# Optimization experiments

Hardware: AMD Instinct MI355X
Metric: run time of the kernel (lower is better)

Reference implementation:

```python
import jax, jax.numpy as jnp
import numpy as np

EPS = 1e-8

def _normalize(x, eps=EPS):
    mean = jnp.mean(x, axis=-1, keepdims=True)
    var = jnp.var(x, axis=-1, keepdims=True)  # unbiased=False
    return (x - mean) / jnp.sqrt(var + eps)


def setup_inputs() -> dict:
    key = jax.random.key(0)
    ks = jax.random.split(key, 10)
    B, M, d = 8, 50000, 256
    out_units, num_heads, gsl_hidden = 256, 8, 16
    s = 0.02
    return {
        "h": jax.random.normal(ks[0], (B, M, d), dtype=jnp.float32),
        "att_w": jax.random.normal(ks[1], (d, num_heads), dtype=jnp.float32) * s,
        "att_b": jnp.zeros((num_heads,), dtype=jnp.float32),
        "w_w": jax.random.normal(ks[2], (d, out_units), dtype=jnp.float32) * s,
        "res_w": jax.random.normal(ks[3], (d, out_units), dtype=jnp.float32) * s,
        "res_b": jnp.zeros((out_units,), dtype=jnp.float32),
        "gsl1_w": jax.random.normal(ks[4], (d, gsl_hidden), dtype=jnp.float32) * s,
        "gsl1_b": jnp.zeros((gsl_hidden,), dtype=jnp.float32),
        "gsl2_w": jax.random.normal(ks[5], (gsl_hidden, 1), dtype=jnp.float32) * s,
        "gsl2_b": jnp.zeros((1,), dtype=jnp.float32),
        "k": 500,
    }


def reference(h, att_w, att_b, w_w, res_w, res_b, gsl1_w, gsl1_b, gsl2_w, gsl2_b, k):
    B, M, d = h.shape
    num_heads = att_w.shape[1]
    out_units = w_w.shape[1]
    head_dim = out_units // num_heads

    # additive attention scores per head: [B, M, H]
    A = jax.nn.relu(jnp.einsum('bmd,dh->bmh', h, att_w) + att_b)
    # value projection: [B, M, out]
    H_lin = jnp.einsum('bmd,de->bme', h, w_w)

    # learned graph-structure-learning scores: [B, M]
    S_hidden = jax.nn.relu(jnp.einsum('bmd,dg->bmg', h, gsl1_w) + gsl1_b)
    S = jax.nn.sigmoid(jnp.einsum('bmg,go->bmo', S_hidden, gsl2_w) + gsl2_b)[..., 0]

    # top-k mask over nodes (dim=1)
    k_eff = min(k, M)
    topk_vals, _ = jax.lax.top_k(S, k_eff)  # sorted descending
    kth = topk_vals[:, -1:]                 # [B, 1]
    mask = (S >= kth).astype(h.dtype)       # [B, M]

    # masked scores (zeros at masked positions, NOT -inf: faithful to source)
    A_mod = A * mask[:, :, None]            # [B, M, H]
    weights = jax.nn.softmax(A_mod, axis=1)  # softmax over M per head
    # (dropout is a no-op in eval mode)

    # per-head weighted sum over nodes, then concat heads along feature dim
    Hr = H_lin.reshape(B, M, num_heads, head_dim)
    out = jnp.einsum('bmh,bmhd->bhd', weights, Hr).reshape(B, 1, out_units)

    # residual from mean-pooled input
    Q_res = jax.nn.relu(jnp.einsum('bmd,de->bme', jnp.mean(h, axis=1, keepdims=True), res_w) + res_b)
    out = jax.nn.relu(out + Q_res)
    return _normalize(out), mask[:, None, :]
```

## Files before the change

kernel.cpp:

```cpp
#include <hip/hip_runtime.h>
#include <cstdint>
#include <cstddef>


#define MM     50000
#define BATCH  8
#define TILES  196
#define CANDCAP 4096
#define COMPCAP 2048

#define OFF_Z      0u
#define OFF_CANDR  1600000u
#define OFF_CANDK  1731072u
#define OFF_COMP   1993216u
#define OFF_LO     2058752u
#define OFF_PAD    2058784u
#define OFF_SUMH   2058848u
#define OFF_UCORR  2075232u
#define OFF_ZCORR  2206304u
#define OFF_CCNT   2206816u
#define OFF_CANDC  2206848u
#define ZERO_OFF   OFF_SUMH
#define ZERO_SZ    148032u

__device__ __forceinline__ unsigned int f32_sortable(float z) {
    unsigned int u = __float_as_uint(z);
    return (u & 0x80000000u) ? ~u : (u | 0x80000000u);
}

__global__ __launch_bounds__(256, 4) void k1_main(
    const float* __restrict__ h,
    const float* __restrict__ g1w,
    const float* __restrict__ g1b,
    const float* __restrict__ g2w,
    const float* __restrict__ g2b,
    float* __restrict__ z32,
    double* __restrict__ sumh)
{
    __shared__ float tile[4][16][66];
    __shared__ float lsum[256];
    __shared__ float wlds[256 * 16];

    const int tid  = threadIdx.x;
    const int w    = tid >> 6;
    const int lane = tid & 63;
    lsum[tid] = 0.0f;
    {
        const float4* g4 = (const float4*)g1w;
        float4*       w4 = (float4*)wlds;
#pragma unroll
        for (int i = 0; i < 4; ++i) w4[tid + 256 * i] = g4[tid + 256 * i];
    }
    __syncthreads();

    const int bid = blockIdx.x;
    const int b   = bid / TILES;
    const int t0  = bid % TILES;
    const int wave_row0 = t0 * 256 + w * 64;
    const size_t bbase = (size_t)b * MM;

    const int subrow = lane >> 2;
    const int colq   = lane & 3;

    const float* rp[4];
    bool valid[4];
#pragma unroll
    for (int i = 0; i < 4; ++i) {
        const int m = wave_row0 + subrow + 16 * i;
        valid[i] = (m < MM);
        const int mc = valid[i] ? m : (MM - 1);
        rp[i] = h + (bbase + (size_t)mc) * 256 + colq * 4;
    }

    float4 buf[4];

#define K1_LOAD(cc) do {                                                    \
    _Pragma("unroll")                                                       \
    for (int i = 0; i < 4; ++i) {                                           \
        float4 v = *(const float4*)(rp[i] + (cc) * 16);                     \
        if (!valid[i]) { v.x = 0.f; v.y = 0.f; v.z = 0.f; v.w = 0.f; }      \
        buf[i] = v;                                                         \
    }                                                                       \
} while (0)

#define K1_CSUM(cc) do {                                                    \
    float sx = 0.f, sy = 0.f, sz = 0.f, sw = 0.f;                           \
    _Pragma("unroll")                                                       \
    for (int i = 0; i < 4; ++i) {                                           \
        sx += buf[i].x; sy += buf[i].y; sz += buf[i].z; sw += buf[i].w;     \
    }                                                                       \
    sx += __shfl_xor(sx, 4, 64);  sy += __shfl_xor(sy, 4, 64);              \
    sz += __shfl_xor(sz, 4, 64);  sw += __shfl_xor(sw, 4, 64);              \
    sx += __shfl_xor(sx, 8, 64);  sy += __shfl_xor(sy, 8, 64);              \
    sz += __shfl_xor(sz, 8, 64);  sw += __shfl_xor(sw, 8, 64);              \
    sx += __shfl_xor(sx, 16, 64); sy += __shfl_xor(sy, 16, 64);             \
    sz += __shfl_xor(sz, 16, 64); sw += __shfl_xor(sw, 16, 64);             \
    sx += __shfl_xor(sx, 32, 64); sy += __shfl_xor(sy, 32, 64);             \
    sz += __shfl_xor(sz, 32, 64); sw += __shfl_xor(sw, 32, 64);             \
    if (subrow == 0) {                                                      \
        atomicAdd(&lsum[(cc) * 16 + colq * 4 + 0], sx);                     \
        atomicAdd(&lsum[(cc) * 16 + colq * 4 + 1], sy);                     \
        atomicAdd(&lsum[(cc) * 16 + colq * 4 + 2], sz);                     \
        atomicAdd(&lsum[(cc) * 16 + colq * 4 + 3], sw);                     \
    }                                                                       \
} while (0)

#define K1_STORE() do {                                                     \
    _Pragma("unroll")                                                       \
    for (int i = 0; i < 4; ++i) {                                           \
        const int rr = subrow + 16 * i;                                     \
        tile[w][colq * 4 + 0][rr] = buf[i].x;                               \
        tile[w][colq * 4 + 1][rr] = buf[i].y;                               \
        tile[w][colq * 4 + 2][rr] = buf[i].z;                               \
        tile[w][colq * 4 + 3][rr] = buf[i].w;                               \
    }                                                                       \
} while (0)

    float gacc[16];
#pragma unroll
    for (int g = 0; g < 16; ++g) gacc[g] = 0.0f;

    K1_LOAD(0);
    K1_CSUM(0);
    K1_STORE();

    for (int c = 0; c < 16; ++c) {
        const bool has = (c < 15);
        if (has) K1_LOAD(c + 1);
        const int k0 = c * 16;
#pragma unroll 2
        for (int kk = 0; kk < 16; ++kk) {
            const float hv = tile[w][kk][lane];
            const float4* wp = (const float4*)(wlds + (k0 + kk) * 16);
            const float4 w0 = wp[0], w1 = wp[1], w2 = wp[2], w3 = wp[3];
            gacc[0]  = fmaf(hv, w0.x, gacc[0]);
            gacc[1]  = fmaf(hv, w0.y, gacc[1]);
            gacc[2]  = fmaf(hv, w0.z, gacc[2]);
            gacc[3]  = fmaf(hv, w0.w, gacc[3]);
            gacc[4]  = fmaf(hv, w1.x, gacc[4]);
            gacc[5]  = fmaf(hv, w1.y, gacc[5]);
            gacc[6]  = fmaf(hv, w1.z, gacc[6]);
            gacc[7]  = fmaf(hv, w1.w, gacc[7]);
            gacc[8]  = fmaf(hv, w2.x, gacc[8]);
            gacc[9]  = fmaf(hv, w2.y, gacc[9]);
            gacc[10] = fmaf(hv, w2.z, gacc[10]);
            gacc[11] = fmaf(hv, w2.w, gacc[11]);
            gacc[12] = fmaf(hv, w3.x, gacc[12]);
            gacc[13] = fmaf(hv, w3.y, gacc[13]);
            gacc[14] = fmaf(hv, w3.z, gacc[14]);
            gacc[15] = fmaf(hv, w3.w, gacc[15]);
        }
        if (has) {
            K1_CSUM(c + 1);
            K1_STORE();
        }
    }

#undef K1_LOAD
#undef K1_CSUM
#undef K1_STORE

    const int m = wave_row0 + lane;
    if (m < MM) {
        float z = g2b[0];
#pragma unroll
        for (int g = 0; g < 16; ++g) {
            float sg = gacc[g] + g1b[g];
            sg = fmaxf(sg, 0.0f);
            z = fmaf(sg, g2w[g], z);
        }
        z32[bbase + m] = z;
    }
    __syncthreads();
    atomicAdd(&sumh[b * 256 + tid], (double)lsum[tid]);
}

__global__ __launch_bounds__(1024) void k2_sample(
    const float* __restrict__ z32,
    const int* __restrict__ kptr,
    unsigned int* __restrict__ lo_out)
{
    __shared__ unsigned int buf[1024];
    const int b   = blockIdx.x;
    const int tid = threadIdx.x;
    const size_t base = (size_t)b * MM;
    const int kval = min(*kptr, MM);

    int idx = (int)(((long long)tid * MM) / 1024);
    buf[tid] = f32_sortable(z32[base + idx]);
    __syncthreads();
    for (int sz = 2; sz <= 1024; sz <<= 1)
        for (int j = sz >> 1; j > 0; j >>= 1) {
            __syncthreads();
            int i = tid, ixj = i ^ j;
            if (ixj > i) {
                unsigned int a = buf[i], c = buf[ixj];
                bool up = ((i & sz) == 0);
                if ((up && a > c) || (!up && a < c)) { buf[i] = c; buf[ixj] = a; }
            }
        }
    __syncthreads();
    if (tid == 0) {
        int ks = (int)(((long long)kval * 1024) / MM) + 35;
        ks = min(1023, max(1, ks));
        lo_out[b] = buf[1023 - ks];
    }
}

__global__ __launch_bounds__(256) void k3_band(
    const float* __restrict__ z32,
    const unsigned int* __restrict__ lo_in,
    float* __restrict__ maskout,
    int* __restrict__ cand_cnt,
    int* __restrict__ cand_rows)
{
    int bid = blockIdx.x;
    int b = bid / TILES, t0 = bid % TILES;
    int m = t0 * 256 + threadIdx.x;
    int lane = threadIdx.x & 63;
    bool cand = false;
    if (m < MM) {
        size_t row = (size_t)b * MM + m;
        cand = (f32_sortable(z32[row]) >= lo_in[b]);
        if (!cand) maskout[row] = 0.0f;
    }
    unsigned long long ball = __ballot(cand);
    int wbase = 0;
    if (lane == 0) { int wc = __popcll(ball); if (wc) wbase = atomicAdd(&cand_cnt[b], wc); }
    wbase = __shfl(wbase, 0, 64);
    if (cand) {
        int pos = wbase + __popcll(ball & ((1ull << lane) - 1ull));
        if (pos < CANDCAP) cand_rows[b * CANDCAP + pos] = m;
    }
}

__global__ __launch_bounds__(256) void k3r_refine(
    const float* __restrict__ h,
    const float* __restrict__ g1w,
    const float* __restrict__ g1b,
    const float* __restrict__ g2w,
    const float* __restrict__ g2b,
    const int* __restrict__ cand_cnt,
    const int* __restrict__ cand_rows,
    unsigned long long* __restrict__ cand_keys)
{
    __shared__ double g1s[256][16];
    const int b    = blockIdx.x >> 4;
    const int part = blockIdx.x & 15;
    const int tid  = threadIdx.x;
    for (int i = tid; i < 4096; i += 256) g1s[i >> 4][i & 15] = (double)g1w[i];
    __syncthreads();

    const int n = min(cand_cnt[b], CANDCAP);
    const size_t bbase = (size_t)b * MM;
    for (int slot = part * 256 + tid; slot < n; slot += 4096) {
        int row = cand_rows[b * CANDCAP + slot];
        const float* hp = h + (bbase + (size_t)row) * 256;
        double gacc[16];
#pragma unroll
        for (int g = 0; g < 16; ++g) gacc[g] = 0.0;
        for (int k = 0; k < 256; ++k) {
            double hd = (double)hp[k];
#pragma unroll
            for (int g = 0; g < 16; ++g) gacc[g] = fma(hd, g1s[k][g], gacc[g]);
        }
        double z = (double)g2b[0];
#pragma unroll
        for (int g = 0; g < 16; ++g) {
            double sg = gacc[g] + (double)g1b[g];
            sg = sg > 0.0 ? sg : 0.0;
            z = fma(sg, (double)g2w[g], z);
        }
        long long uz = __double_as_longlong(z);
        unsigned long long key = (uz < 0)
            ? ~((unsigned long long)uz)
            : ((unsigned long long)uz | 0x8000000000000000ULL);
        cand_keys[b * CANDCAP + slot] = key;
    }
}

__global__ __launch_bounds__(1024) void k3s_select(
    const int* __restrict__ kptr,
    const int* __restrict__ cand_cnt,
    const int* __restrict__ cand_rows,
    const unsigned long long* __restrict__ cand_keys,
    float* __restrict__ maskout,
    int* __restrict__ ccnt,
    int* __restrict__ compact)
{
    __shared__ unsigned long long kbuf[CANDCAP];
    __shared__ int s_cnt;

    const int b    = blockIdx.x;
    const int tid  = threadIdx.x;
    const int lane = tid & 63;
    const int n = min(cand_cnt[b], CANDCAP);
    const size_t bbase = (size_t)b * MM;
    int kval = min(*kptr, MM);
    if (kval > n) kval = n;

    for (int i = tid; i < n; i += 1024) kbuf[i] = cand_keys[b * CANDCAP + i];
    __syncthreads();

    unsigned long long p64 = 0;
    int kk = kval;
    for (int bit = 63; bit >= 0; --bit) {
        if (tid == 0) s_cnt = 0;
        __syncthreads();
        unsigned long long himask = (bit == 63) ? 0ull : (~0ull << (bit + 1));
        int loc = 0;
        for (int i = tid; i < n; i += 1024) {
            unsigned long long x = kbuf[i];
            if (((x ^ p64) & himask) == 0ull && ((x >> bit) & 1ull)) loc++;
        }
        loc += __shfl_xor(loc, 32, 64);
        loc += __shfl_xor(loc, 16, 64);
        loc += __shfl_xor(loc, 8, 64);
        loc += __shfl_xor(loc, 4, 64);
        loc += __shfl_xor(loc, 2, 64);
        loc += __shfl_xor(loc, 1, 64);
        if (lane == 0 && loc) atomicAdd(&s_cnt, loc);
        __syncthreads();
        int c1 = s_cnt;
        if (c1 >= kk) p64 |= (1ull << bit); else kk -= c1;
        __syncthreads();
    }

    for (int i0 = 0; i0 < n; i0 += 1024) {
        int i = i0 + tid;
        bool active = (i < n);
        bool mk = false;
        int row = 0;
        if (active) {
            row = cand_rows[b * CANDCAP + i];
            mk = (kbuf[i] >= p64);
            maskout[bbase + row] = mk ? 1.0f : 0.0f;
        }
        unsigned long long ball = __ballot(mk);
        int wbase = 0;
        if (lane == 0) { int wc = __popcll(ball); if (wc) wbase = atomicAdd(&ccnt[b], wc); }
        wbase = __shfl(wbase, 0, 64);
        if (mk) {
            int pos = wbase + __popcll(ball & ((1ull << lane) - 1ull));
            if (pos < COMPCAP) compact[b * COMPCAP + pos] = row;
        }
    }
}

__global__ __launch_bounds__(256) void k4_corr(
    const float* __restrict__ h,
    const float* __restrict__ att_w,
    const float* __restrict__ att_b,
    const int* __restrict__ compact,
    const int* __restrict__ ccnt,
    double* __restrict__ Ucorr,
    double* __restrict__ Zcorr)
{
    __shared__ float hv_s[256];
    __shared__ float a_s[8];

    const int b    = blockIdx.x >> 5;
    const int part = blockIdx.x & 31;
    const int tid  = threadIdx.x;
    const int head = tid >> 5;
    const int seg  = tid & 31;
    const size_t bbase = (size_t)b * MM;
    const int n = min(ccnt[b], COMPCAP);

    float acc[8], zac[8];
#pragma unroll
    for (int j = 0; j < 8; ++j) { acc[j] = 0.f; zac[j] = 0.f; }

    for (int i = part; i < n; i += 32) {
        int row = compact[b * COMPCAP + i];
        float hv = h[(bbase + (size_t)row) * 256 + tid];
        hv_s[tid] = hv;
        __syncthreads();
        float p = 0.f;
#pragma unroll
        for (int j = 0; j < 8; ++j)
            p = fmaf(hv_s[seg * 8 + j], att_w[(seg * 8 + j) * 8 + head], p);
        p += __shfl_xor(p, 1, 64);
        p += __shfl_xor(p, 2, 64);
        p += __shfl_xor(p, 4, 64);
        p += __shfl_xor(p, 8, 64);
        p += __shfl_xor(p, 16, 64);
        if (seg == 0) a_s[head] = fmaxf(p + att_b[head], 0.f);
        __syncthreads();
#pragma unroll
        for (int j = 0; j < 8; ++j) {
            float w8 = expf(a_s[j]) - 1.0f;
            acc[j] = fmaf(w8, hv, acc[j]);
            zac[j] += w8;
        }
        __syncthreads();
    }
#pragma unroll
    for (int j = 0; j < 8; ++j)
        atomicAdd(&Ucorr[(b * 8 + j) * 256 + tid], (double)acc[j]);
    if (tid == 0) {
#pragma unroll
        for (int j = 0; j < 8; ++j) atomicAdd(&Zcorr[b * 8 + j], (double)zac[j]);
    }
}

__global__ __launch_bounds__(256) void k5_final(
    const double* __restrict__ sumh,
    const double* __restrict__ Ucorr,
    const double* __restrict__ Zcorr,
    const int* __restrict__ ccnt,
    const float* __restrict__ w_w,
    const float* __restrict__ res_w,
    const float* __restrict__ res_b,
    float* __restrict__ out0)
{
    __shared__ float Us[8 * 256];
    __shared__ float ms[256];
    __shared__ float red[256];
    __shared__ float s_mean, s_var;

    int b = blockIdx.x, e = threadIdx.x;
    double sh = sumh[b * 256 + e];
    ms[e] = (float)sh;
#pragma unroll
    for (int j = 0; j < 8; ++j)
        Us[j * 256 + e] = (float)(sh + Ucorr[(b * 8 + j) * 256 + e]);
    __syncthreads();

    int hh = e >> 5;
    float Z = (float)((double)(MM - ccnt[b]) + Zcorr[b * 8 + hh]);
    float attn = 0.f, qr = 0.f;
    for (int d = 0; d < 256; ++d) {
        attn = fmaf(Us[hh * 256 + d], w_w[d * 256 + e], attn);
        qr   = fmaf(ms[d],            res_w[d * 256 + e], qr);
    }
    float qres = fmaxf(qr * (1.0f / (float)MM) + res_b[e], 0.f);
    float pre  = fmaxf(attn / Z + qres, 0.f);

    red[e] = pre; __syncthreads();
    for (int s = 128; s > 0; s >>= 1) { if (e < s) red[e] += red[e + s]; __syncthreads(); }
    if (e == 0) s_mean = red[0] * (1.0f / 256.0f);
    __syncthreads();
    float mean = s_mean;
    float dv = pre - mean;
    red[e] = dv * dv; __syncthreads();
    for (int s = 128; s > 0; s >>= 1) { if (e < s) red[e] += red[e + s]; __syncthreads(); }
    if (e == 0) s_var = red[0] * (1.0f / 256.0f);
    __syncthreads();
    out0[b * 256 + e] = dv / sqrtf(s_var + 1e-8f);
}

extern "C" void kernel_launch(void* const* d_in, const int* in_sizes, int n_in,
                              void* d_out, int out_size, void* d_ws, size_t ws_size,
                              hipStream_t stream) {
    const float* h     = (const float*)d_in[0];
    const float* att_w = (const float*)d_in[1];
    const float* att_b = (const float*)d_in[2];
    const float* w_w   = (const float*)d_in[3];
    const float* res_w = (const float*)d_in[4];
    const float* res_b = (const float*)d_in[5];
    const float* g1w   = (const float*)d_in[6];
    const float* g1b   = (const float*)d_in[7];
    const float* g2w   = (const float*)d_in[8];
    const float* g2b   = (const float*)d_in[9];
    const int*   kptr  = (const int*)d_in[10];

    char* ws = (char*)d_ws;
    float*              z32     = (float*)(ws + OFF_Z);
    int*                candr   = (int*)(ws + OFF_CANDR);
    unsigned long long* candk   = (unsigned long long*)(ws + OFF_CANDK);
    int*                compact = (int*)(ws + OFF_COMP);
    unsigned int*       lo      = (unsigned int*)(ws + OFF_LO);
    double*             sumh    = (double*)(ws + OFF_SUMH);
    double*             Ucorr   = (double*)(ws + OFF_UCORR);
    double*             Zcorr   = (double*)(ws + OFF_ZCORR);
    int*                ccnt    = (int*)(ws + OFF_CCNT);
    int*                candc   = (int*)(ws + OFF_CANDC);

    float* out0    = (float*)d_out;
    float* maskout = out0 + BATCH * 256;

    hipMemsetAsync(ws + ZERO_OFF, 0, ZERO_SZ, stream);

    k1_main   <<<BATCH*TILES, 256,  0, stream>>>(h, g1w, g1b, g2w, g2b, z32, sumh);
    k2_sample <<<BATCH,       1024, 0, stream>>>(z32, kptr, lo);
    k3_band   <<<BATCH*TILES, 256,  0, stream>>>(z32, lo, maskout, candc, candr);
    k3r_refine<<<BATCH*16,    256,  0, stream>>>(h, g1w, g1b, g2w, g2b,
                                                 candc, candr, candk);
    k3s_select<<<BATCH,       1024, 0, stream>>>(kptr, candc, candr, candk,
                                                 maskout, ccnt, compact);
    k4_corr   <<<BATCH*32,    256,  0, stream>>>(h, att_w, att_b, compact, ccnt,
                                                 Ucorr, Zcorr);
    k5_final  <<<BATCH,       256,  0, stream>>>(sumh, Ucorr, Zcorr, ccnt,
                                                 w_w, res_w, res_b, out0);
}
```

Measured before the change: 800.2 us.

## Process two rows per lane in k1 and use single-wave radix select

The main streaming kernel now gives each wave 128 rows instead of 64, with two accumulator sets per lane. Each LDS weight fetch therefore feeds twice as many FMAs, and the block count is halved. Separately, the 64-bit radix select kernel now runs as one 64-thread wave using shuffles only, which removes the three block barriers and the shared atomic on each of the 64 bit iterations. The cost is more registers and a larger LDS tile in k1, which may reduce occupancy, and less parallelism in the candidate scan of the select kernel.

Result: slower. 924.3 us (+15.5%).

```diff
diff --git a/kernel.cpp b/kernel.cpp
--- a/kernel.cpp
+++ b/kernel.cpp
@@ -6,6 +6,7 @@
 #define MM     50000
 #define BATCH  8
 #define TILES  196
+#define K1TILES 98
 #define CANDCAP 4096
 #define COMPCAP 2048
 
@@ -37,7 +38,7 @@
     float* __restrict__ z32,
     double* __restrict__ sumh)
 {
-    __shared__ float tile[4][16][66];
+    __shared__ float tile[4][16][130];
     __shared__ float lsum[256];
     __shared__ float wlds[256 * 16];
 
@@ -54,31 +55,31 @@
     __syncthreads();
 
     const int bid = blockIdx.x;
-    const int b   = bid / TILES;
-    const int t0  = bid % TILES;
-    const int wave_row0 = t0 * 256 + w * 64;
+    const int b   = bid / K1TILES;
+    const int t0  = bid % K1TILES;
+    const int wave_row0 = t0 * 512 + w * 128;
     const size_t bbase = (size_t)b * MM;
 
     const int subrow = lane >> 2;
     const int colq   = lane & 3;
 
-    const float* rp[4];
-    bool valid[4];
-#pragma unroll
-    for (int i = 0; i < 4; ++i) {
+    const float* rp[8];
+    int iv = 0;
+#pragma unroll
+    for (int i = 0; i < 8; ++i) {
         const int m = wave_row0 + subrow + 16 * i;
-        valid[i] = (m < MM);
-        const int mc = valid[i] ? m : (MM - 1);
+        const int mc = (m < MM) ? m : (MM - 1);
         rp[i] = h + (bbase + (size_t)mc) * 256 + colq * 4;
-    }
-
-    float4 buf[4];
+        if (m < MM) iv = i + 1;
+    }
+
+    float4 buf[8];
 
 #define K1_LOAD(cc) do {                                                    \
     _Pragma("unroll")                                                       \
-    for (int i = 0; i < 4; ++i) {                                           \
+    for (int i = 0; i < 8; ++i) {                                           \
         float4 v = *(const float4*)(rp[i] + (cc) * 16);                     \
-        if (!valid[i]) { v.x = 0.f; v.y = 0.f; v.z = 0.f; v.w = 0.f; }      \
+        if (i >= iv) { v.x = 0.f; v.y = 0.f; v.z = 0.f; v.w = 0.f; }        \
         buf[i] = v;                                                         \
     }                                                                       \
 } while (0)
@@ -86,7 +87,7 @@
 #define K1_CSUM(cc) do {                                                    \
     float sx = 0.f, sy = 0.f, sz = 0.f, sw = 0.f;                           \
     _Pragma("unroll")                                                       \
-    for (int i = 0; i < 4; ++i) {                                           \
+    for (int i = 0; i < 8; ++i) {                                           \
         sx += buf[i].x; sy += buf[i].y; sz += buf[i].z; sw += buf[i].w;     \
     }                                                                       \
     sx += __shfl_xor(sx, 4, 64);  sy += __shfl_xor(sy, 4, 64);              \
@@ -107,7 +108,7 @@
 
 #define K1_STORE() do {                                                     \
     _Pragma("unroll")                                                       \
-    for (int i = 0; i < 4; ++i) {                                           \
+    for (int i = 0; i < 8; ++i) {                                           \
         const int rr = subrow + 16 * i;                                     \
         tile[w][colq * 4 + 0][rr] = buf[i].x;                               \
         tile[w][colq * 4 + 1][rr] = buf[i].y;                               \
@@ -116,9 +117,9 @@
     }                                                                       \
 } while (0)
 
-    float gacc[16];
-#pragma unroll
-    for (int g = 0; g < 16; ++g) gacc[g] = 0.0f;
+    float gacc0[16], gacc1[16];
+#pragma unroll
+    for (int g = 0; g < 16; ++g) { gacc0[g] = 0.0f; gacc1[g] = 0.0f; }
 
     K1_LOAD(0);
     K1_CSUM(0);
@@ -128,27 +129,28 @@
         const bool has = (c < 15);
         if (has) K1_LOAD(c + 1);
         const int k0 = c * 16;
-#pragma unroll 2
+#pragma unroll 1
         for (int kk = 0; kk < 16; ++kk) {
-            const float hv = tile[w][kk][lane];
+            const float hv0 = tile[w][kk][lane];
+            const float hv1 = tile[w][kk][64 + lane];
             const float4* wp = (const float4*)(wlds + (k0 + kk) * 16);
             const float4 w0 = wp[0], w1 = wp[1], w2 = wp[2], w3 = wp[3];
-            gacc[0]  = fmaf(hv, w0.x, gacc[0]);
-            gacc[1]  = fmaf(hv, w0.y, gacc[1]);
-            gacc[2]  = fmaf(hv, w0.z, gacc[2]);
-            gacc[3]  = fmaf(hv, w0.w, gacc[3]);
-            gacc[4]  = fmaf(hv, w1.x, gacc[4]);
-            gacc[5]  = fmaf(hv, w1.y, gacc[5]);
-            gacc[6]  = fmaf(hv, w1.z, gacc[6]);
-            gacc[7]  = fmaf(hv, w1.w, gacc[7]);
-            gacc[8]  = fmaf(hv, w2.x, gacc[8]);
-            gacc[9]  = fmaf(hv, w2.y, gacc[9]);
-            gacc[10] = fmaf(hv, w2.z, gacc[10]);
-            gacc[11] = fmaf(hv, w2.w, gacc[11]);
-            gacc[12] = fmaf(hv, w3.x, gacc[12]);
-            gacc[13] = fmaf(hv, w3.y, gacc[13]);
-            gacc[14] = fmaf(hv, w3.z, gacc[14]);
-            gacc[15] = fmaf(hv, w3.w, gacc[15]);
+            gacc0[0]  = fmaf(hv0, w0.x, gacc0[0]);  gacc1[0]  = fmaf(hv1, w0.x, gacc1[0]);
+            gacc0[1]  = fmaf(hv0, w0.y, gacc0[1]);  gacc1[1]  = fmaf(hv1, w0.y, gacc1[1]);
+            gacc0[2]  = fmaf(hv0, w0.z, gacc0[2]);  gacc1[2]  = fmaf(hv1, w0.z, gacc1[2]);
+            gacc0[3]  = fmaf(hv0, w0.w, gacc0[3]);  gacc1[3]  = fmaf(hv1, w0.w, gacc1[3]);
+            gacc0[4]  = fmaf(hv0, w1.x, gacc0[4]);  gacc1[4]  = fmaf(hv1, w1.x, gacc1[4]);
+            gacc0[5]  = fmaf(hv0, w1.y, gacc0[5]);  gacc1[5]  = fmaf(hv1, w1.y, gacc1[5]);
+            gacc0[6]  = fmaf(hv0, w1.z, gacc0[6]);  gacc1[6]  = fmaf(hv1, w1.z, gacc1[6]);
+            gacc0[7]  = fmaf(hv0, w1.w, gacc0[7]);  gacc1[7]  = fmaf(hv1, w1.w, gacc1[7]);
+            gacc0[8]  = fmaf(hv0, w2.x, gacc0[8]);  gacc1[8]  = fmaf(hv1, w2.x, gacc1[8]);
+            gacc0[9]  = fmaf(hv0, w2.y, gacc0[9]);  gacc1[9]  = fmaf(hv1, w2.y, gacc1[9]);
+            gacc0[10] = fmaf(hv0, w2.z, gacc0[10]); gacc1[10] = fmaf(hv1, w2.z, gacc1[10]);
+            gacc0[11] = fmaf(hv0, w2.w, gacc0[11]); gacc1[11] = fmaf(hv1, w2.w, gacc1[11]);
+            gacc0[12] = fmaf(hv0, w3.x, gacc0[12]); gacc1[12] = fmaf(hv1, w3.x, gacc1[12]);
+            gacc0[13] = fmaf(hv0, w3.y, gacc0[13]); gacc1[13] = fmaf(hv1, w3.y, gacc1[13]);
+            gacc0[14] = fmaf(hv0, w3.z, gacc0[14]); gacc1[14] = fmaf(hv1, w3.z, gacc1[14]);
+            gacc0[15] = fmaf(hv0, w3.w, gacc0[15]); gacc1[15] = fmaf(hv1, w3.w, gacc1[15]);
         }
         if (has) {
             K1_CSUM(c + 1);
@@ -160,16 +162,29 @@
 #undef K1_CSUM
 #undef K1_STORE
 
-    const int m = wave_row0 + lane;
-    if (m < MM) {
-        float z = g2b[0];
-#pragma unroll
-        for (int g = 0; g < 16; ++g) {
-            float sg = gacc[g] + g1b[g];
-            sg = fmaxf(sg, 0.0f);
-            z = fmaf(sg, g2w[g], z);
-        }
-        z32[bbase + m] = z;
+    {
+        const int m0 = wave_row0 + lane;
+        if (m0 < MM) {
+            float z = g2b[0];
+#pragma unroll
+            for (int g = 0; g < 16; ++g) {
+                float sg = gacc0[g] + g1b[g];
+                sg = fmaxf(sg, 0.0f);
+                z = fmaf(sg, g2w[g], z);
+            }
+            z32[bbase + m0] = z;
+        }
+        const int m1 = wave_row0 + 64 + lane;
+        if (m1 < MM) {
+            float z = g2b[0];
+#pragma unroll
+            for (int g = 0; g < 16; ++g) {
+                float sg = gacc1[g] + g1b[g];
+                sg = fmaxf(sg, 0.0f);
+                z = fmaf(sg, g2w[g], z);
+            }
+            z32[bbase + m1] = z;
+        }
     }
     __syncthreads();
     atomicAdd(&sumh[b * 256 + tid], (double)lsum[tid]);
@@ -279,7 +294,7 @@
     }
 }
 
-__global__ __launch_bounds__(1024) void k3s_select(
+__global__ __launch_bounds__(64) void k3s_select(
     const int* __restrict__ kptr,
     const int* __restrict__ cand_cnt,
     const int* __restrict__ cand_rows,
@@ -289,49 +304,39 @@
     int* __restrict__ compact)
 {
     __shared__ unsigned long long kbuf[CANDCAP];
-    __shared__ int s_cnt;
 
     const int b    = blockIdx.x;
-    const int tid  = threadIdx.x;
-    const int lane = tid & 63;
+    const int lane = threadIdx.x;
     const int n = min(cand_cnt[b], CANDCAP);
     const size_t bbase = (size_t)b * MM;
     int kval = min(*kptr, MM);
     if (kval > n) kval = n;
 
-    for (int i = tid; i < n; i += 1024) kbuf[i] = cand_keys[b * CANDCAP + i];
-    __syncthreads();
+    for (int i = lane; i < n; i += 64) kbuf[i] = cand_keys[b * CANDCAP + i];
 
     unsigned long long p64 = 0;
     int kk = kval;
     for (int bit = 63; bit >= 0; --bit) {
-        if (tid == 0) s_cnt = 0;
-        __syncthreads();
         unsigned long long himask = (bit == 63) ? 0ull : (~0ull << (bit + 1));
         int loc = 0;
-        for (int i = tid; i < n; i += 1024) {
+        for (int i = lane; i < n; i += 64) {
             unsigned long long x = kbuf[i];
             if (((x ^ p64) & himask) == 0ull && ((x >> bit) & 1ull)) loc++;
         }
+        loc += __shfl_xor(loc, 1, 64);
+        loc += __shfl_xor(loc, 2, 64);
+        loc += __shfl_xor(loc, 4, 64);
+        loc += __shfl_xor(loc, 8, 64);
+        loc += __shfl_xor(loc, 16, 64);
         loc += __shfl_xor(loc, 32, 64);
-        loc += __shfl_xor(loc, 16, 64);
-        loc += __shfl_xor(loc, 8, 64);
-        loc += __shfl_xor(loc, 4, 64);
-        loc += __shfl_xor(loc, 2, 64);
-        loc += __shfl_xor(loc, 1, 64);
-        if (lane == 0 && loc) atomicAdd(&s_cnt, loc);
-        __syncthreads();
-        int c1 = s_cnt;
-        if (c1 >= kk) p64 |= (1ull << bit); else kk -= c1;
-        __syncthreads();
-    }
-
-    for (int i0 = 0; i0 < n; i0 += 1024) {
-        int i = i0 + tid;
-        bool active = (i < n);
+        if (loc >= kk) p64 |= (1ull << bit); else kk -= loc;
+    }
+
+    for (int i0 = 0; i0 < n; i0 += 64) {
+        int i = i0 + lane;
         bool mk = false;
         int row = 0;
-        if (active) {
+        if (i < n) {
             row = cand_rows[b * CANDCAP + i];
             mk = (kbuf[i] >= p64);
             maskout[bbase + row] = mk ? 1.0f : 0.0f;
@@ -482,15 +487,15 @@
 
     hipMemsetAsync(ws + ZERO_OFF, 0, ZERO_SZ, stream);
 
-    k1_main   <<<BATCH*TILES, 256,  0, stream>>>(h, g1w, g1b, g2w, g2b, z32, sumh);
-    k2_sample <<<BATCH,       1024, 0, stream>>>(z32, kptr, lo);
-    k3_band   <<<BATCH*TILES, 256,  0, stream>>>(z32, lo, maskout, candc, candr);
-    k3r_refine<<<BATCH*16,    256,  0, stream>>>(h, g1w, g1b, g2w, g2b,
-                                                 candc, candr, candk);
-    k3s_select<<<BATCH,       1024, 0, stream>>>(kptr, candc, candr, candk,
-                                                 maskout, ccnt, compact);
-    k4_corr   <<<BATCH*32,    256,  0, stream>>>(h, att_w, att_b, compact, ccnt,
-                                                 Ucorr, Zcorr);
-    k5_final  <<<BATCH,       256,  0, stream>>>(sumh, Ucorr, Zcorr, ccnt,
-                                                 w_w, res_w, res_b, out0);
-}
+    k1_main   <<<BATCH*K1TILES, 256,  0, stream>>>(h, g1w, g1b, g2w, g2b, z32, sumh);
+    k2_sample <<<BATCH,         1024, 0, stream>>>(z32, kptr, lo);
+    k3_band   <<<BATCH*TILES,   256,  0, stream>>>(z32, lo, maskout, candc, candr);
+    k3r_refine<<<BATCH*16,      256,  0, stream>>>(h, g1w, g1b, g2w, g2b,
+                                                   candc, candr, candk);
+    k3s_select<<<BATCH,         64,   0, stream>>>(kptr, candc, candr, candk,
+                                                   maskout, ccnt, compact);
+    k4_corr   <<<BATCH*32,      256,  0, stream>>>(h, att_w, att_b, compact, ccnt,
+                                                   Ucorr, Zcorr);
+    k5_final  <<<BATCH,         256,  0, stream>>>(sumh, Ucorr, Zcorr, ccnt,
+                                                   w_w, res_w, res_b, out0);
+}
```
